# Optimization experiments

Measured on AMD Instinct MI355X. Metric: run time of the kernel, lower is better.

The kernel has to match this reference:

```python
import jax, jax.numpy as jnp
import numpy as np

E = 768
H = 12
DK = E // H
B = 4
S = 2048
EPS = 1e-5


def setup_inputs() -> dict:
    key = jax.random.key(0)
    ks = jax.random.split(key, 8)
    # xavier_uniform bound for square [E, E] weight
    bound = float(np.sqrt(6.0 / (E + E)))
    def xavier(k):
        return jax.random.uniform(k, (E, E), jnp.float32, -bound, bound)
    return {
        "query": jax.random.normal(ks[0], (B, S, E), jnp.float32),
        "key": jax.random.normal(ks[1], (B, S, E), jnp.float32),
        "value": jax.random.normal(ks[2], (B, S, E), jnp.float32),
        "enc_attn_mask": jax.random.randint(ks[3], (B, S, S), 0, 2).astype(bool),
        "Wq": xavier(ks[4]),
        "Wk": xavier(ks[5]),
        "Wv": xavier(ks[6]),
        "Wo": xavier(ks[7]),
    }


def reference(query, key, value, enc_attn_mask, Wq, Wk, Wv, Wo):
    b, s, _ = query.shape
    # projections (nn.Linear: y = x @ W.T), split heads -> [b, h, s, dk]
    Q = (query @ Wq.T).reshape(b, s, H, DK).transpose(0, 2, 1, 3)
    K = (key @ Wk.T).reshape(b, s, H, DK).transpose(0, 2, 1, 3)
    V = (value @ Wv.T).reshape(b, s, H, DK).transpose(0, 2, 1, 3)
    # scaled dot-product attention with boolean mask (True -> -1e9)
    scores = jnp.einsum("bhqd,bhkd->bhqk", Q, K) / np.sqrt(DK).astype(np.float32)
    scores = jnp.where(enc_attn_mask[:, None, :, :], jnp.float32(-1e9), scores)
    attn = jax.nn.softmax(scores, axis=-1)
    context = jnp.einsum("bhqk,bhkd->bhqd", attn, V)
    context = context.transpose(0, 2, 1, 3).reshape(b, s, E)
    out = context @ Wo.T + query  # residual
    # fresh nn.LayerNorm(E): weight=1, bias=0, eps=1e-5
    mean = jnp.mean(out, axis=-1, keepdims=True)
    var = jnp.var(out, axis=-1, keepdims=True)
    return (out - mean) * jax.lax.rsqrt(var + EPS)
```

## Files before the change

kernel.cpp:

```cpp
#include <hip/hip_runtime.h>
#include <stdint.h>
#include <stddef.h>

#define HN   12
#define SN   2048
#define EN   768
#define DKN  64
#define BATCH 4
#define MROWS 8192

typedef short bf16x8 __attribute__((ext_vector_type(8)));
typedef float f32x4 __attribute__((ext_vector_type(4)));

__device__ __forceinline__ unsigned short f2bf(float f) {
  union { float f; unsigned u; } x; x.f = f;
  unsigned r = x.u + 0x7fffu + ((x.u >> 16) & 1u);
  return (unsigned short)(r >> 16);
}

#if __has_builtin(__builtin_amdgcn_cvt_pk_bf16_f32)
typedef __bf16 bf16v2 __attribute__((ext_vector_type(2)));
__device__ __forceinline__ unsigned pk_bf16(float a, float b) {
  union { bf16v2 v; unsigned u; } c;
  c.v = __builtin_amdgcn_cvt_pk_bf16_f32(a, b);
  return c.u;
}
#else
__device__ __forceinline__ unsigned pk_bf16(float a, float b) {
  return (unsigned)f2bf(a) | ((unsigned)f2bf(b) << 16);
}
#endif

#define GLD_LDS16(gptr, lptr) \
  __builtin_amdgcn_global_load_lds((const __attribute__((address_space(1))) void*)(gptr), \
                                   (__attribute__((address_space(3))) void*)(lptr), 16, 0, 0)

#define NBIG4 1572864
#define NW4   147456
__global__ __launch_bounds__(256) void cvt_all(const float* __restrict__ q,
                                               const float* __restrict__ k,
                                               const float* __restrict__ v,
                                               const float* __restrict__ wq,
                                               const float* __restrict__ wk,
                                               const float* __restrict__ wv,
                                               const float* __restrict__ wo,
                                               unsigned short* __restrict__ dst) {
  const int i = blockIdx.x * 256 + threadIdx.x;
  const float* src;
  int off;
  if (i < 3 * NBIG4) {
    const int r = i / NBIG4;
    src = (r == 0) ? q : (r == 1) ? k : v;
    off = i - r * NBIG4;
  } else {
    const int j = i - 3 * NBIG4;
    const int r = j / NW4;
    src = (r == 0) ? wq : (r == 1) ? wk : (r == 2) ? wv : wo;
    off = j - r * NW4;
  }
  float4 val = ((const float4*)src)[off];
  ushort4 o;
  o.x = f2bf(val.x); o.y = f2bf(val.y); o.z = f2bf(val.z); o.w = f2bf(val.w);
  ((ushort4*)dst)[i] = o;
}

__global__ __launch_bounds__(256) void mask_pack(const int* __restrict__ mask,
                                                 unsigned long long* __restrict__ out) {
  const int row = (blockIdx.x * 256 + threadIdx.x) >> 6;
  const int lane = threadIdx.x & 63;
  const int* mrow = mask + (size_t)row * SN;
  unsigned long long* orow = out + (size_t)row * 32;
  for (int kt = 0; kt < 32; ++kt) {
    int v = mrow[kt * 64 + lane];
    unsigned long long bm = __ballot(v != 0);
    if (lane == 0) orow[kt] = bm;
  }
}

__global__ __launch_bounds__(256) void gemm_qkv(const unsigned short* __restrict__ Xb,
                                                const unsigned short* __restrict__ Wb,
                                                unsigned short* __restrict__ Ob,
                                                float qscale) {
  __shared__ unsigned short As[128 * 32];
  __shared__ unsigned short Bs[128 * 32];
  const int tid  = threadIdx.x;
  const int wave = tid >> 6;
  const int lane = tid & 63;
  const int quad = lane >> 4;
  const int l16  = lane & 15;
  const int bm = blockIdx.x;
  const int bn = blockIdx.y;
  const int z  = blockIdx.z;
  const int wm = wave & 1;
  const int wn = wave >> 1;

  const unsigned short* X = Xb + (size_t)z * MROWS * EN;
  const unsigned short* W = Wb + (size_t)z * EN * EN;
  unsigned short* O = Ob + (size_t)z * MROWS * EN;

  f32x4 acc[4][4] = {};
  const int srow = lane >> 2;
  const int schk = lane & 3;

  for (int bk = 0; bk < 24; ++bk) {
    __syncthreads();
#pragma unroll
    for (int r = 0; r < 2; ++r) {
      const int rowblk = r * 64 + wave * 16;
      GLD_LDS16(X + (size_t)(bm * 128 + rowblk + srow) * EN + bk * 32 + schk * 8,
                As + rowblk * 32);
      GLD_LDS16(W + (size_t)(bn * 128 + rowblk + srow) * EN + bk * 32 + schk * 8,
                Bs + rowblk * 32);
    }
    __syncthreads();

    bf16x8 af[4], bfr[4];
#pragma unroll
    for (int mt = 0; mt < 4; ++mt)
      af[mt] = *(const bf16x8*)&As[(wm * 64 + mt * 16 + l16) * 32 + quad * 8];
#pragma unroll
    for (int nt = 0; nt < 4; ++nt)
      bfr[nt] = *(const bf16x8*)&Bs[(wn * 64 + nt * 16 + l16) * 32 + quad * 8];
#pragma unroll
    for (int mt = 0; mt < 4; ++mt)
#pragma unroll
      for (int nt = 0; nt < 4; ++nt)
        acc[mt][nt] = __builtin_amdgcn_mfma_f32_16x16x32_bf16(af[mt], bfr[nt], acc[mt][nt], 0, 0, 0);
  }

  const int m0 = bm * 128 + wm * 64;
  const int n0 = bn * 128 + wn * 64;
  const float scale = (z == 0) ? qscale : 1.0f;

  if (z < 2) {
#pragma unroll
    for (int mt = 0; mt < 4; ++mt) {
#pragma unroll
      for (int nt = 0; nt < 4; ++nt) {
        const int n = n0 + nt * 16 + l16;
        const int h = n >> 6, d = n & 63;
#pragma unroll
        for (int r = 0; r < 4; ++r) {
          const int m = m0 + mt * 16 + quad * 4 + r;
          const int b = m >> 11, s = m & 2047;
          O[((size_t)(b * HN + h) * SN + s) * DKN + d] = f2bf(acc[mt][nt][r] * scale);
        }
      }
    }
  } else {
#pragma unroll
    for (int mt = 0; mt < 4; ++mt) {
#pragma unroll
      for (int nt = 0; nt < 4; ++nt) {
        const int n = n0 + nt * 16 + l16;
        const int h = n >> 6, d = n & 63;
        const int m = m0 + mt * 16 + quad * 4;
        const int b = m >> 11, s = m & 2047;
        ushort4 pk;
        pk.x = f2bf(acc[mt][nt][0]);
        pk.y = f2bf(acc[mt][nt][1]);
        pk.z = f2bf(acc[mt][nt][2]);
        pk.w = f2bf(acc[mt][nt][3]);
        *(ushort4*)&O[((size_t)(b * HN + h) * DKN + d) * SN + s] = pk;
      }
    }
  }
}

__global__ __launch_bounds__(256) void gemm_out(const unsigned short* __restrict__ X,
                                                const unsigned short* __restrict__ W,
                                                float* __restrict__ O,
                                                const float* __restrict__ residual) {
  __shared__ unsigned short As[128 * 32];
  __shared__ unsigned short Bs[128 * 32];
  const int tid  = threadIdx.x;
  const int wave = tid >> 6;
  const int lane = tid & 63;
  const int quad = lane >> 4;
  const int l16  = lane & 15;
  const int bm = blockIdx.x;
  const int bn = blockIdx.y;
  const int wm = wave & 1;
  const int wn = wave >> 1;

  f32x4 acc[4][4] = {};
  const int srow = lane >> 2;
  const int schk = lane & 3;

  for (int bk = 0; bk < 24; ++bk) {
    __syncthreads();
#pragma unroll
    for (int r = 0; r < 2; ++r) {
      const int rowblk = r * 64 + wave * 16;
      GLD_LDS16(X + (size_t)(bm * 128 + rowblk + srow) * EN + bk * 32 + schk * 8,
                As + rowblk * 32);
      GLD_LDS16(W + (size_t)(bn * 128 + rowblk + srow) * EN + bk * 32 + schk * 8,
                Bs + rowblk * 32);
    }
    __syncthreads();

    bf16x8 af[4], bfr[4];
#pragma unroll
    for (int mt = 0; mt < 4; ++mt)
      af[mt] = *(const bf16x8*)&As[(wm * 64 + mt * 16 + l16) * 32 + quad * 8];
#pragma unroll
    for (int nt = 0; nt < 4; ++nt)
      bfr[nt] = *(const bf16x8*)&Bs[(wn * 64 + nt * 16 + l16) * 32 + quad * 8];
#pragma unroll
    for (int mt = 0; mt < 4; ++mt)
#pragma unroll
      for (int nt = 0; nt < 4; ++nt)
        acc[mt][nt] = __builtin_amdgcn_mfma_f32_16x16x32_bf16(af[mt], bfr[nt], acc[mt][nt], 0, 0, 0);
  }

  const int m0 = bm * 128 + wm * 64;
  const int n0 = bn * 128 + wn * 64;
#pragma unroll
  for (int mt = 0; mt < 4; ++mt) {
#pragma unroll
    for (int nt = 0; nt < 4; ++nt) {
      const int n = n0 + nt * 16 + l16;
#pragma unroll
      for (int r = 0; r < 4; ++r) {
        const int m = m0 + mt * 16 + quad * 4 + r;
        const size_t idx = (size_t)m * EN + n;
        O[idx] = acc[mt][nt][r] + residual[idx];
      }
    }
  }
}

__global__ __launch_bounds__(256, 4) void attn_kernel(const unsigned short* __restrict__ Q,
                                                      const unsigned short* __restrict__ K,
                                                      const unsigned short* __restrict__ Vt,
                                                      const unsigned* __restrict__ Mbits32,
                                                      unsigned short* __restrict__ Ctx) {
  __shared__ __align__(16) unsigned char LDSBUF[64 * 68 * 4];
  __shared__ float lpart[2][2][16];
  unsigned short* Ks = (unsigned short*)LDSBUF;
  unsigned short* Vs = (unsigned short*)(LDSBUF + 8192);
  float* Cmb = (float*)LDSBUF;

  const int tid  = threadIdx.x;
  const int wave = tid >> 6, lane = tid & 63;
  const int quad = lane >> 4, l16 = lane & 15;
  const int qhalf = wave >> 1, kh = wave & 1;
  const int qt = blockIdx.x, bh = blockIdx.y;
  const int b = bh / HN, h = bh - b * HN;

  const unsigned short* Qp = Q + (size_t)bh * SN * DKN;
  const unsigned short* Kp = K + (size_t)bh * SN * DKN;
  const unsigned short* Vp = Vt + (size_t)bh * DKN * SN;

  const int srow = lane >> 3;
  const int schk = lane & 7;
  const int swsrc = (schk ^ srow) * 8;
  const int c0 = (quad ^ (l16 & 7)) * 8;
  const int cv = (((kh << 2) + quad) ^ (l16 & 7)) * 8;
  const int shq = 31 - quad * 8;

  const int pw = wave * 8 + srow;
  const int yk = (((pw >> 2) & 3) << 3) + ((pw >> 4) << 2) + (pw & 3);

  bf16x8 bq[2][2];
#pragma unroll
  for (int qg = 0; qg < 2; ++qg) {
    const int R = qt * 64 + qhalf * 32 + qg * 16 + l16;
    bq[qg][0] = *(const bf16x8*)(Qp + (size_t)R * DKN + quad * 8);
    bq[qg][1] = *(const bf16x8*)(Qp + (size_t)R * DKN + 32 + quad * 8);
  }

  const unsigned* M0 = Mbits32 + ((size_t)(b * SN + qt * 64 + qhalf * 32 + l16)) * 64 + kh;

  f32x4 o_acc[2][4] = {};
  f32x4 o_l[2] = {};
  bf16x8 ones;
#pragma unroll
  for (int i = 0; i < 8; ++i) ones[i] = (short)0x3F80;

  for (int kt = 0; kt < 32; ++kt) {
    __syncthreads();
    GLD_LDS16(Kp + (size_t)(kt * 64 + yk) * DKN + swsrc,              Ks + (wave * 8) * 64);
    GLD_LDS16(Kp + (size_t)(kt * 64 + 32 + yk) * DKN + swsrc,         Ks + (32 + wave * 8) * 64);
    GLD_LDS16(Vp + (size_t)(wave * 8 + srow) * SN + kt * 64 + swsrc,      Vs + (wave * 8) * 64);
    GLD_LDS16(Vp + (size_t)(32 + wave * 8 + srow) * SN + kt * 64 + swsrc, Vs + (32 + wave * 8) * 64);
    const unsigned m0w = M0[kt * 2];
    const unsigned m1w = M0[kt * 2 + 16 * 64];
    __syncthreads();

    bf16x8 ak[2][2];
#pragma unroll
    for (int mt = 0; mt < 2; ++mt) {
      const int base = (kh * 32 + mt * 16 + l16) * 64;
      ak[mt][0] = *(const bf16x8*)&Ks[base + c0];
      ak[mt][1] = *(const bf16x8*)&Ks[base + (c0 ^ 32)];
    }

    f32x4 st[2][2];
#pragma unroll
    for (int qg = 0; qg < 2; ++qg)
#pragma unroll
      for (int mt = 0; mt < 2; ++mt) {
        f32x4 c = {};
        c = __builtin_amdgcn_mfma_f32_16x16x32_bf16(ak[mt][0], bq[qg][0], c, 0, 0, 0);
        c = __builtin_amdgcn_mfma_f32_16x16x32_bf16(ak[mt][1], bq[qg][1], c, 0, 0, 0);
        st[qg][mt] = c;
      }

    bf16x8 av[4];
#pragma unroll
    for (int dt = 0; dt < 4; ++dt)
      av[dt] = *(const bf16x8*)&Vs[(dt * 16 + l16) * 64 + cv];

#pragma unroll
    for (int qg = 0; qg < 2; ++qg) {
      const unsigned w = qg ? m1w : m0w;
      float p[8];
#pragma unroll
      for (int mt = 0; mt < 2; ++mt)
#pragma unroll
        for (int r = 0; r < 4; ++r) {
          const float sv = ((int)(w << (shq - mt * 4 - r)) < 0) ? -1e9f : st[qg][mt][r];
          p[mt * 4 + r] = __builtin_exp2f(sv);
        }
      union { unsigned u[4]; bf16x8 v; } pk;
      pk.u[0] = pk_bf16(p[0], p[1]);
      pk.u[1] = pk_bf16(p[2], p[3]);
      pk.u[2] = pk_bf16(p[4], p[5]);
      pk.u[3] = pk_bf16(p[6], p[7]);
      o_l[qg] = __builtin_amdgcn_mfma_f32_16x16x32_bf16(ones, pk.v, o_l[qg], 0, 0, 0);
#pragma unroll
      for (int dt = 0; dt < 4; ++dt)
        o_acc[qg][dt] = __builtin_amdgcn_mfma_f32_16x16x32_bf16(av[dt], pk.v, o_acc[qg][dt], 0, 0, 0);
    }
  }

  __syncthreads();
  if (kh == 1) {
#pragma unroll
    for (int qg = 0; qg < 2; ++qg) {
#pragma unroll
      for (int dt = 0; dt < 4; ++dt)
        *(f32x4*)&Cmb[(qhalf * 32 + qg * 16 + l16) * 68 + dt * 16 + quad * 4] = o_acc[qg][dt];
      if (quad == 0) lpart[qhalf][qg][l16] = o_l[qg][0];
    }
  }
  __syncthreads();
  if (kh == 0) {
#pragma unroll
    for (int qg = 0; qg < 2; ++qg) {
      const float l = o_l[qg][0] + lpart[qhalf][qg][l16];
      const float inv = 1.0f / l;
      const int R = qt * 64 + qhalf * 32 + qg * 16 + l16;
      unsigned short* Crow = Ctx + (size_t)(b * SN + R) * EN + h * 64;
#pragma unroll
      for (int dt = 0; dt < 4; ++dt) {
        const f32x4 part = *(const f32x4*)&Cmb[(qhalf * 32 + qg * 16 + l16) * 68 + dt * 16 + quad * 4];
        ushort4 wst;
        wst.x = f2bf((o_acc[qg][dt][0] + part[0]) * inv);
        wst.y = f2bf((o_acc[qg][dt][1] + part[1]) * inv);
        wst.z = f2bf((o_acc[qg][dt][2] + part[2]) * inv);
        wst.w = f2bf((o_acc[qg][dt][3] + part[3]) * inv);
        *(ushort4*)&Crow[dt * 16 + quad * 4] = wst;
      }
    }
  }
}

__global__ __launch_bounds__(256) void ln_kernel(const float* __restrict__ X,
                                                 float* __restrict__ Y) {
  const int row = blockIdx.x;
  const int t = threadIdx.x;
  const float* xr = X + (size_t)row * EN;
  float v[3];
  float s = 0.f, ss = 0.f;
#pragma unroll
  for (int i = 0; i < 3; ++i) {
    v[i] = xr[t + i * 256];
    s += v[i];
    ss += v[i] * v[i];
  }
#pragma unroll
  for (int off = 1; off < 64; off <<= 1) {
    s += __shfl_xor(s, off, 64);
    ss += __shfl_xor(ss, off, 64);
  }
  __shared__ float ws_s[4], ws_q[4];
  const int wave = t >> 6, lane = t & 63;
  if (lane == 0) { ws_s[wave] = s; ws_q[wave] = ss; }
  __syncthreads();
  s = ws_s[0] + ws_s[1] + ws_s[2] + ws_s[3];
  ss = ws_q[0] + ws_q[1] + ws_q[2] + ws_q[3];
  const float mean = s * (1.0f / EN);
  const float var = ss * (1.0f / EN) - mean * mean;
  const float rstd = rsqrtf(var + 1e-5f);
  float* yr = Y + (size_t)row * EN;
#pragma unroll
  for (int i = 0; i < 3; ++i) yr[t + i * 256] = (v[i] - mean) * rstd;
}

extern "C" void kernel_launch(void* const* d_in, const int* in_sizes, int n_in,
                              void* d_out, int out_size, void* d_ws, size_t ws_size,
                              hipStream_t stream) {
  (void)in_sizes; (void)n_in; (void)out_size; (void)ws_size;
  const float* query = (const float*)d_in[0];
  const float* key_i = (const float*)d_in[1];
  const float* value = (const float*)d_in[2];
  const int*   mask  = (const int*)d_in[3];
  const float* Wq = (const float*)d_in[4];
  const float* Wk = (const float*)d_in[5];
  const float* Wv = (const float*)d_in[6];
  const float* Wo = (const float*)d_in[7];

  const size_t NBIG = (size_t)MROWS * EN;
  const size_t NW   = (size_t)EN * EN;

  unsigned short* Xq16 = (unsigned short*)d_ws;
  unsigned short* Wq16 = Xq16 + 3 * NBIG;
  unsigned short* Wo16 = Wq16 + 3 * NW;
  unsigned short* Q16  = Wo16 + NW;
  unsigned short* K16  = Q16 + NBIG;
  unsigned short* Vt16 = K16 + NBIG;
  unsigned short* Ctx16 = Vt16 + NBIG;
  float* OutF = (float*)(Ctx16 + NBIG);
  unsigned long long* Mbits = (unsigned long long*)OutF;

  mask_pack<<<MROWS / 4, 256, 0, stream>>>(mask, Mbits);

  const int ncvt = 3 * NBIG4 + 4 * NW4;
  cvt_all<<<ncvt / 256, 256, 0, stream>>>(query, key_i, value, Wq, Wk, Wv, Wo, Xq16);

  gemm_qkv<<<dim3(MROWS / 128, EN / 128, 3), 256, 0, stream>>>(
      Xq16, Wq16, Q16, 0.125f * 1.44269504088896f);

  attn_kernel<<<dim3(SN / 64, BATCH * HN), 256, 0, stream>>>(
      Q16, K16, Vt16, (const unsigned*)Mbits, Ctx16);

  gemm_out<<<dim3(MROWS / 128, EN / 128), 256, 0, stream>>>(Ctx16, Wo16, OutF, query);

  ln_kernel<<<MROWS, 256, 0, stream>>>(OutF, (float*)d_out);
}
```

Measured before the change: 375.1 us.

## Load K/V fragments directly from global in attention; fuse mask packing into conversion

```diff
diff --git a/kernel.cpp b/kernel.cpp
--- a/kernel.cpp
+++ b/kernel.cpp
@@ -37,6 +37,7 @@
 
 #define NBIG4 1572864
 #define NW4   147456
+#define NCVTB 20736
 __global__ __launch_bounds__(256) void cvt_all(const float* __restrict__ q,
                                                const float* __restrict__ k,
                                                const float* __restrict__ v,
@@ -44,7 +45,21 @@
                                                const float* __restrict__ wk,
                                                const float* __restrict__ wv,
                                                const float* __restrict__ wo,
-                                               unsigned short* __restrict__ dst) {
+                                               unsigned short* __restrict__ dst,
+                                               const int* __restrict__ mask,
+                                               unsigned long long* __restrict__ mout) {
+  if (blockIdx.x >= NCVTB) {
+    const int row = ((blockIdx.x - NCVTB) * 256 + threadIdx.x) >> 6;
+    const int lane = threadIdx.x & 63;
+    const int* mrow = mask + (size_t)row * SN;
+    unsigned long long* orow = mout + (size_t)row * 32;
+    for (int kt = 0; kt < 32; ++kt) {
+      int mv = mrow[kt * 64 + lane];
+      unsigned long long bm = __ballot(mv != 0);
+      if (lane == 0) orow[kt] = bm;
+    }
+    return;
+  }
   const int i = blockIdx.x * 256 + threadIdx.x;
   const float* src;
   int off;
@@ -62,19 +77,6 @@
   ushort4 o;
   o.x = f2bf(val.x); o.y = f2bf(val.y); o.z = f2bf(val.z); o.w = f2bf(val.w);
   ((ushort4*)dst)[i] = o;
-}
-
-__global__ __launch_bounds__(256) void mask_pack(const int* __restrict__ mask,
-                                                 unsigned long long* __restrict__ out) {
-  const int row = (blockIdx.x * 256 + threadIdx.x) >> 6;
-  const int lane = threadIdx.x & 63;
-  const int* mrow = mask + (size_t)row * SN;
-  unsigned long long* orow = out + (size_t)row * 32;
-  for (int kt = 0; kt < 32; ++kt) {
-    int v = mrow[kt * 64 + lane];
-    unsigned long long bm = __ballot(v != 0);
-    if (lane == 0) orow[kt] = bm;
-  }
 }
 
 __global__ __launch_bounds__(256) void gemm_qkv(const unsigned short* __restrict__ Xb,
@@ -235,11 +237,8 @@
                                                       const unsigned short* __restrict__ Vt,
                                                       const unsigned* __restrict__ Mbits32,
                                                       unsigned short* __restrict__ Ctx) {
-  __shared__ __align__(16) unsigned char LDSBUF[64 * 68 * 4];
+  __shared__ __align__(16) float Cmb[64 * 68];
   __shared__ float lpart[2][2][16];
-  unsigned short* Ks = (unsigned short*)LDSBUF;
-  unsigned short* Vs = (unsigned short*)(LDSBUF + 8192);
-  float* Cmb = (float*)LDSBUF;
 
   const int tid  = threadIdx.x;
   const int wave = tid >> 6, lane = tid & 63;
@@ -252,15 +251,11 @@
   const unsigned short* Kp = K + (size_t)bh * SN * DKN;
   const unsigned short* Vp = Vt + (size_t)bh * DKN * SN;
 
-  const int srow = lane >> 3;
-  const int schk = lane & 7;
-  const int swsrc = (schk ^ srow) * 8;
-  const int c0 = (quad ^ (l16 & 7)) * 8;
-  const int cv = (((kh << 2) + quad) ^ (l16 & 7)) * 8;
   const int shq = 31 - quad * 8;
 
-  const int pw = wave * 8 + srow;
-  const int yk = (((pw >> 2) & 3) << 3) + ((pw >> 4) << 2) + (pw & 3);
+  const int krow0 = kh * 32 + ((l16 >> 2) << 3) + (l16 & 3);
+  const unsigned short* Kb = Kp + (size_t)krow0 * DKN + quad * 8;
+  const unsigned short* Vb = Vp + (size_t)l16 * SN + kh * 32 + quad * 8;
 
   bf16x8 bq[2][2];
 #pragma unroll
@@ -279,22 +274,21 @@
   for (int i = 0; i < 8; ++i) ones[i] = (short)0x3F80;
 
   for (int kt = 0; kt < 32; ++kt) {
-    __syncthreads();
-    GLD_LDS16(Kp + (size_t)(kt * 64 + yk) * DKN + swsrc,              Ks + (wave * 8) * 64);
-    GLD_LDS16(Kp + (size_t)(kt * 64 + 32 + yk) * DKN + swsrc,         Ks + (32 + wave * 8) * 64);
-    GLD_LDS16(Vp + (size_t)(wave * 8 + srow) * SN + kt * 64 + swsrc,      Vs + (wave * 8) * 64);
-    GLD_LDS16(Vp + (size_t)(32 + wave * 8 + srow) * SN + kt * 64 + swsrc, Vs + (32 + wave * 8) * 64);
+    const unsigned short* Kt = Kb + (size_t)kt * 64 * DKN;
+    bf16x8 ak[2][2];
+#pragma unroll
+    for (int mt = 0; mt < 2; ++mt) {
+      ak[mt][0] = *(const bf16x8*)(Kt + mt * 4 * DKN);
+      ak[mt][1] = *(const bf16x8*)(Kt + mt * 4 * DKN + 32);
+    }
+    const unsigned short* Vtk = Vb + kt * 64;
+    bf16x8 av[4];
+#pragma unroll
+    for (int dt = 0; dt < 4; ++dt)
+      av[dt] = *(const bf16x8*)(Vtk + (size_t)dt * 16 * SN);
+
     const unsigned m0w = M0[kt * 2];
     const unsigned m1w = M0[kt * 2 + 16 * 64];
-    __syncthreads();
-
-    bf16x8 ak[2][2];
-#pragma unroll
-    for (int mt = 0; mt < 2; ++mt) {
-      const int base = (kh * 32 + mt * 16 + l16) * 64;
-      ak[mt][0] = *(const bf16x8*)&Ks[base + c0];
-      ak[mt][1] = *(const bf16x8*)&Ks[base + (c0 ^ 32)];
-    }
 
     f32x4 st[2][2];
 #pragma unroll
@@ -306,11 +300,6 @@
         c = __builtin_amdgcn_mfma_f32_16x16x32_bf16(ak[mt][1], bq[qg][1], c, 0, 0, 0);
         st[qg][mt] = c;
       }
-
-    bf16x8 av[4];
-#pragma unroll
-    for (int dt = 0; dt < 4; ++dt)
-      av[dt] = *(const bf16x8*)&Vs[(dt * 16 + l16) * 64 + cv];
 
 #pragma unroll
     for (int qg = 0; qg < 2; ++qg) {
@@ -425,10 +414,8 @@
   float* OutF = (float*)(Ctx16 + NBIG);
   unsigned long long* Mbits = (unsigned long long*)OutF;
 
-  mask_pack<<<MROWS / 4, 256, 0, stream>>>(mask, Mbits);
-
-  const int ncvt = 3 * NBIG4 + 4 * NW4;
-  cvt_all<<<ncvt / 256, 256, 0, stream>>>(query, key_i, value, Wq, Wk, Wv, Wo, Xq16);
+  cvt_all<<<NCVTB + MROWS / 4, 256, 0, stream>>>(query, key_i, value, Wq, Wk, Wv, Wo,
+                                                 Xq16, mask, Mbits);
 
   gemm_qkv<<<dim3(MROWS / 128, EN / 128, 3), 256, 0, stream>>>(
       Xq16, Wq16, Q16, 0.125f * 1.44269504088896f);
```

After: 499.8 us. 33.2% more time.
